# Kernel tuning notes

Measured on AMD Instinct MI355X. Metric: run time of the kernel, lower is better.

## Reference

```python
import jax, jax.numpy as jnp
from jax import lax
import numpy as np


def _conv2d(x, w, b, pad):
    # x: NCHW, w: OIHW
    o = lax.conv_general_dilated(x, w, window_strides=(1, 1),
                                 padding=[(pad, pad), (pad, pad)],
                                 dimension_numbers=('NCHW', 'OIHW', 'NCHW'))
    return o + b[None, :, None, None]


def _maxpool(x, kh, kw):
    return lax.reduce_window(x, -jnp.inf, lax.max,
                             window_dimensions=(1, 1, kh, kw),
                             window_strides=(1, 1, kh, kw),
                             padding='VALID')


def _l2norm(x, axis):
    n = jnp.sqrt(jnp.sum(x * x, axis=axis, keepdims=True))
    return x / jnp.maximum(n, 1e-12)


def setup_inputs() -> dict:
    key = jax.random.key(0)
    ks = jax.random.split(key, 12)
    d = {}
    d['x'] = jax.random.normal(ks[0], (16, 128, 40, 200), dtype=jnp.float32)
    d['cluster_centers'] = jax.random.uniform(ks[1], (64, 128), dtype=jnp.float32)
    d['conv_w'] = jax.random.normal(ks[2], (64, 128, 1, 1), dtype=jnp.float32) * 0.05
    d['conv_b'] = jax.random.normal(ks[3], (64,), dtype=jnp.float32) * 0.05
    d['w1'] = jax.random.normal(ks[4], (256, 128, 5, 5), dtype=jnp.float32) * 0.02
    d['b1'] = jax.random.normal(ks[5], (256,), dtype=jnp.float32) * 0.02
    d['w2'] = jax.random.normal(ks[6], (512, 256, 5, 5), dtype=jnp.float32) * 0.02
    d['b2'] = jax.random.normal(ks[7], (512,), dtype=jnp.float32) * 0.02
    d['w3'] = jax.random.normal(ks[8], (1024, 512, 5, 5), dtype=jnp.float32) * 0.02
    d['b3'] = jax.random.normal(ks[9], (1024,), dtype=jnp.float32) * 0.02
    d['mlp_w'] = jax.random.normal(ks[10], (256, 9216), dtype=jnp.float32) * 0.01
    d['mlp_b'] = jax.random.normal(ks[11], (256,), dtype=jnp.float32) * 0.01
    return d


def reference(x, cluster_centers, conv_w, conv_b, w1, b1, w2, b2, w3, b3, mlp_w, mlp_b):
    N, C, H, W = x.shape
    K = conv_w.shape[0]
    P = H * W

    # soft assignment: 1x1 conv -> softmax over cluster axis
    sa = _conv2d(x, conv_w, conv_b, 0).reshape(N, K, P)
    a = jax.nn.softmax(sa, axis=1)                      # [N, K, P]

    x_flat = x.reshape(N, C, P)
    # sum_p a[n,k,p] * (x[n,c,p] - centers[k,c])  -- algebraically equal to
    # the explicit NxKxCxP residual tensor, computed without materializing it.
    vlad = jnp.einsum('nkp,ncp->nkc', a, x_flat) \
           - a.sum(axis=-1)[:, :, None] * cluster_centers[None, :, :]
    vlad = _l2norm(vlad, axis=2)                        # intra-norm per cluster
    vlad = _l2norm(vlad.reshape(N, K * C), axis=1)      # [N, K*C]

    # CNN branch
    h = _conv2d(x, w1, b1, 2)
    h = jnp.where(h >= 0, h, 0.2 * h)                   # LeakyReLU(0.2)
    h = _maxpool(h, 2, 2)
    h = _conv2d(h, w2, b2, 2)
    h = jnp.where(h >= 0, h, 0.2 * h)
    h = _maxpool(h, 4, 4)
    h = _conv2d(h, w3, b3, 2)
    h = _maxpool(h, 5, 25)                              # -> [N, 1024, 1, 1]
    x_feat = _l2norm(h.reshape(N, -1), axis=1)          # [N, 1024]

    feat = jnp.concatenate([vlad, x_feat], axis=1)      # [N, 9216]
    out = feat @ mlp_w.T + mlp_b
    return _l2norm(out, axis=1)
```

## Files before the change

kernel.cpp:

```cpp
#include <hip/hip_runtime.h>
#include <math.h>

#define K_ 64
#define C_ 128
#define NB 16
#define P_ 8000

typedef float f32x4 __attribute__((ext_vector_type(4)));
typedef short s16x8 __attribute__((ext_vector_type(8)));

__device__ __forceinline__ short f2bf(float v) {
    unsigned u = __float_as_uint(v);
    u += 0x7FFFu + ((u >> 16) & 1u);
    return (short)(u >> 16);
}
__device__ __forceinline__ float bf2f(ushort u) { return __uint_as_float(((unsigned)u) << 16); }

__device__ __forceinline__ void stage16(const void* g, void* l) {
    __builtin_amdgcn_global_load_lds(
        (const __attribute__((address_space(1))) void*)g,
        (__attribute__((address_space(3))) void*)l, 16, 0, 0);
}

__global__ void k_transpose_tiled(const float* __restrict__ in, float* __restrict__ out,
                                  int Co, int E)
{
    __shared__ float t[32][33];
    const int e0  = blockIdx.x * 32;
    const int co0 = blockIdx.y * 32;
    for (int i = threadIdx.y; i < 32; i += 8) {
        int co = co0 + i, e = e0 + threadIdx.x;
        t[i][threadIdx.x] = (co < Co && e < E) ? in[(size_t)co * E + e] : 0.f;
    }
    __syncthreads();
    for (int i = threadIdx.y; i < 32; i += 8) {
        int e = e0 + i, co = co0 + threadIdx.x;
        if (e < E && co < Co) out[(size_t)e * Co + co] = t[threadIdx.x][i];
    }
}

__global__ void k_nchw_to_nhwc(const float* __restrict__ in, ushort* __restrict__ out,
                               int C, int P)
{
    __shared__ ushort t[32][33];
    const int n  = blockIdx.z;
    const int p0 = blockIdx.x * 32;
    const int c0 = blockIdx.y * 32;
    for (int i = threadIdx.y; i < 32; i += 8) {
        int c = c0 + i, p = p0 + threadIdx.x;
        t[i][threadIdx.x] = (c < C && p < P) ? (ushort)f2bf(in[((size_t)n * C + c) * P + p]) : 0;
    }
    __syncthreads();
    for (int i = threadIdx.y; i < 32; i += 8) {
        int p = p0 + i, c = c0 + threadIdx.x;
        if (p < P && c < C) out[((size_t)n * P + p) * C + c] = t[threadIdx.x][i];
    }
}

__global__ void k_wprep(const float* __restrict__ w, short* __restrict__ wb,
                        int Co, int Cin, int total)
{
    int idx = blockIdx.x * blockDim.x + threadIdx.x;
    if (idx >= total) return;
    int cl = idx & 31;
    int rest = idx >> 5;
    int co = rest % Co;
    int rest2 = rest / Co;
    int t = rest2 % 25;
    int ck = rest2 / 25;
    float v = w[((size_t)co * Cin + (ck << 5) + cl) * 25 + t];
    wb[idx] = f2bf(v);
}

template<int SR, int NC, int WR, int WC16, int IS3>
__global__ __launch_bounds__(256) void k_conv_mfma(
    const ushort* __restrict__ in, const s16x8* __restrict__ wb,
    const float* __restrict__ bias, ushort* __restrict__ outb, float* __restrict__ outf,
    const ushort* __restrict__ zg,
    int Cin, int Co, int H, int W, int WT, int leaky, int nck, int xpc, int PT)
{
    constexpr int NT   = IS3 ? 8 : (WR * WC16);
    constexpr int TOT  = SR * NC * 4;
    constexpr int TOTP = (TOT + 63) & ~63;
    __shared__ s16x8 xin[TOTP];

    const int tid  = threadIdx.x;
    const int lane = tid & 63;
    const int wid  = tid >> 6;
    const int wm   = wid;
    const int n16  = lane & 15;
    const int g    = lane >> 4;

    const int lid  = blockIdx.x;
    const int xcd  = lid & 7;
    const int rrr  = lid >> 3;
    const int co_blk = xcd / xpc;
    const int posn = rrr * xpc + (xcd % xpc);
    const int n    = posn / PT;
    const int bx   = posn % PT;

    const int h0  = IS3 ? 0 : (bx / WT) * WR;
    const int w0  = IS3 ? 0 : (bx % WT) * (WC16 * 16);
    const int ks  = IS3 ? bx : 0;
    const int co0 = co_blk * 256;

    int ph[NT], pw[NT];
    if (IS3) {
        #pragma unroll
        for (int nt = 0; nt < NT; ++nt) {
            int pos = nt * 16 + n16;
            int h = pos / 25;
            int w = pos - h * 25;
            if (h > 4) { h = 0; w = 0; }
            ph[nt] = h; pw[nt] = w;
        }
    }

    f32x4 acc[4][NT];
    #pragma unroll
    for (int i = 0; i < 4; ++i)
        #pragma unroll
        for (int j = 0; j < NT; ++j) acc[i][j] = f32x4{0.f, 0.f, 0.f, 0.f};

    const int ck0 = IS3 ? ks * nck : 0;
    const int ckend = ck0 + nck;

    auto stage_input = [&](int ck) {
        for (int c = wid; c * 64 < TOTP; c += 4) {
            int u = c * 64 + lane;
            int row = u / (NC * 4);
            int rem = u - row * (NC * 4);
            int col = rem >> 2;
            int s   = rem & 3;
            int g8  = (s - (col >> 1) - row) & 3;
            int gh = h0 + row - 2, gw = w0 + col - 2;
            const void* src =
                (u < TOT && (unsigned)gh < (unsigned)H && (unsigned)gw < (unsigned)W)
                ? (const void*)(in + ((size_t)(n * H + gh) * W + gw) * Cin + (ck << 5) + (g8 << 3))
                : (const void*)zg;
            stage16(src, (void*)&xin[c * 64]);
        }
    };

    for (int ck = ck0; ck < ckend; ++ck) {
        if (ck != ck0) __syncthreads();
        stage_input(ck);
        __syncthreads();

        const s16x8* wbc = wb + ((size_t)(ck * 25) * Co + co0 + wm * 64 + n16) * 4 + g;

        s16x8 wreg[3][4];
        #pragma unroll
        for (int mt = 0; mt < 4; ++mt) wreg[0][mt] = wbc[mt * 64];
        #pragma unroll
        for (int mt = 0; mt < 4; ++mt) wreg[1][mt] = wbc[(size_t)Co * 4 + mt * 64];

        #pragma unroll
        for (int t = 0; t < 25; ++t) {
            if (t < 23) {
                const s16x8* wn = wbc + (size_t)(t + 2) * Co * 4;
                #pragma unroll
                for (int mt = 0; mt < 4; ++mt) wreg[(t + 2) % 3][mt] = wn[mt * 64];
            }
            const int r = t / 5, s = t - (t / 5) * 5;

            s16x8 bf[NT];
            #pragma unroll
            for (int nt = 0; nt < NT; ++nt) {
                int row, col;
                if (IS3) { row = ph[nt] + r; col = pw[nt] + s; }
                else {
                    int rr = nt / WC16, cc = nt - rr * WC16;
                    row = rr + r;
                    col = cc * 16 + n16 + s;
                }
                bf[nt] = xin[(row * NC + col) * 4 + ((g + (col >> 1) + row) & 3)];
            }
            __builtin_amdgcn_s_setprio(1);
            #pragma unroll
            for (int mt = 0; mt < 4; ++mt)
                #pragma unroll
                for (int nt = 0; nt < NT; ++nt)
                    acc[mt][nt] = __builtin_amdgcn_mfma_f32_16x16x32_bf16(
                        wreg[t % 3][mt], bf[nt], acc[mt][nt], 0, 0, 0);
            __builtin_amdgcn_s_setprio(0);
        }
    }

    if (IS3) {
        #pragma unroll
        for (int mt = 0; mt < 4; ++mt) {
            #pragma unroll
            for (int reg = 0; reg < 4; ++reg) {
                const int co = co0 + wm * 64 + mt * 16 + g * 4 + reg;
                #pragma unroll
                for (int nt = 0; nt < NT; ++nt) {
                    int pos = nt * 16 + n16;
                    if (pos < 125)
                        outf[((size_t)(ks * NB + n) * Co + co) * 125 + pos] = acc[mt][nt][reg];
                }
            }
        }
    } else {
        #pragma unroll
        for (int mt = 0; mt < 4; ++mt) {
            const int cobase = co0 + wm * 64 + mt * 16 + g * 4;
            const float b0 = bias[cobase + 0];
            const float b1 = bias[cobase + 1];
            const float b2 = bias[cobase + 2];
            const float b3 = bias[cobase + 3];
            #pragma unroll
            for (int nt = 0; nt < NT; ++nt) {
                int rr = nt / WC16, cc = nt - rr * WC16;
                int h  = h0 + rr;
                int wp = w0 + cc * 16 + n16;
                if (h < H && wp < W) {
                    float v0 = acc[mt][nt][0] + b0;
                    float v1 = acc[mt][nt][1] + b1;
                    float v2 = acc[mt][nt][2] + b2;
                    float v3 = acc[mt][nt][3] + b3;
                    if (leaky) {
                        v0 = (v0 >= 0.f) ? v0 : 0.2f * v0;
                        v1 = (v1 >= 0.f) ? v1 : 0.2f * v1;
                        v2 = (v2 >= 0.f) ? v2 : 0.2f * v2;
                        v3 = (v3 >= 0.f) ? v3 : 0.2f * v3;
                    }
                    ushort4 pkd;
                    pkd.x = (ushort)f2bf(v0);
                    pkd.y = (ushort)f2bf(v1);
                    pkd.z = (ushort)f2bf(v2);
                    pkd.w = (ushort)f2bf(v3);
                    *(ushort4*)(outb + ((size_t)(n * H + h) * W + wp) * Co + cobase) = pkd;
                }
            }
        }
    }
}

__global__ __launch_bounds__(256) void k_vlad_partial(
    const float* __restrict__ x,
    const float* __restrict__ convw_t,
    const float* __restrict__ convb,
    float* __restrict__ pv,
    float* __restrict__ pa)
{
    __shared__ float xs[C_][64];
    __shared__ float als[64][K_];
    __shared__ float pgsum[4][K_];

    const int tid = threadIdx.x;
    const int chunk = blockIdx.x;
    const int n = blockIdx.y;
    const int p0 = chunk * 64;

    const float* xn = x + (size_t)n * C_ * P_ + p0;
    for (int i = tid; i < C_ * 64; i += 256) {
        int c = i >> 6, pp = i & 63;
        xs[c][pp] = xn[(size_t)c * P_ + pp];
    }
    __syncthreads();

    const int k  = tid & 63;
    const int pg = tid >> 6;

    float sa[16];
    const float bk = convb[k];
    #pragma unroll
    for (int j = 0; j < 16; ++j) sa[j] = bk;
    for (int c = 0; c < C_; ++c) {
        float wv = convw_t[c * K_ + k];
        const float4* xp = (const float4*)&xs[c][pg * 16];
        #pragma unroll
        for (int q = 0; q < 4; ++q) {
            float4 xv = xp[q];
            sa[q*4+0] += wv * xv.x;
            sa[q*4+1] += wv * xv.y;
            sa[q*4+2] += wv * xv.z;
            sa[q*4+3] += wv * xv.w;
        }
    }

    float asum_loc = 0.f;
    #pragma unroll
    for (int j = 0; j < 16; ++j) {
        float m = sa[j];
        for (int d = 32; d >= 1; d >>= 1) m = fmaxf(m, __shfl_xor(m, d));
        float e = __expf(sa[j] - m);
        float s = e;
        for (int d = 32; d >= 1; d >>= 1) s += __shfl_xor(s, d);
        float a = e / s;
        als[pg * 16 + j][k] = a;
        asum_loc += a;
    }
    pgsum[pg][k] = asum_loc;
    __syncthreads();
    if (tid < K_) {
        pa[((size_t)n * 125 + chunk) * K_ + tid] =
            pgsum[0][tid] + pgsum[1][tid] + pgsum[2][tid] + pgsum[3][tid];
    }

    const int q = pg;
    float acc[32];
    #pragma unroll
    for (int j = 0; j < 32; ++j) acc[j] = 0.f;
    for (int p = 0; p < 64; p += 4) {
        float a0 = als[p+0][k], a1 = als[p+1][k], a2 = als[p+2][k], a3 = als[p+3][k];
        #pragma unroll
        for (int j = 0; j < 32; ++j) {
            const float4 xv = *(const float4*)&xs[q*32 + j][p];
            acc[j] += a0*xv.x + a1*xv.y + a2*xv.z + a3*xv.w;
        }
    }
    float* pvp = pv + ((((size_t)n * 125 + chunk) * K_ + k) * C_ + q * 32);
    #pragma unroll
    for (int j = 0; j < 32; ++j) pvp[j] = acc[j];
}

__global__ void k_vlad_reduce(const float* __restrict__ pv, float* __restrict__ vlad_raw)
{
    int idx = blockIdx.x * blockDim.x + threadIdx.x;
    if (idx >= NB * 8192) return;
    int n = idx >> 13;
    int rest = idx & 8191;
    const float* p = pv + (size_t)n * 125 * 8192 + rest;
    float s = 0.f;
    for (int ch = 0; ch < 125; ++ch) s += p[(size_t)ch * 8192];
    vlad_raw[(size_t)n * 8192 + rest] = s;
}

__global__ void k_asum_reduce(const float* __restrict__ pa, float* __restrict__ asum)
{
    int idx = blockIdx.x * blockDim.x + threadIdx.x;
    if (idx >= NB * K_) return;
    const float* p = pa + (size_t)(idx >> 6) * 125 * K_ + (idx & 63);
    float s = 0.f;
    for (int ch = 0; ch < 125; ++ch) s += p[ch * K_];
    asum[idx] = s;
}

__global__ __launch_bounds__(128) void k_vlad_finalize(
    const float* __restrict__ vlad_raw, const float* __restrict__ asum,
    const float* __restrict__ centers, float* __restrict__ feat)
{
    __shared__ float red[2];
    const int k = blockIdx.x, n = blockIdx.y, c = threadIdx.x;
    float v = vlad_raw[((size_t)n * K_ + k) * C_ + c] - asum[n * K_ + k] * centers[k * C_ + c];
    float ss = v * v;
    for (int d = 32; d >= 1; d >>= 1) ss += __shfl_xor(ss, d);
    if ((threadIdx.x & 63) == 0) red[threadIdx.x >> 6] = ss;
    __syncthreads();
    float denom = fmaxf(sqrtf(red[0] + red[1]), 1e-12f);
    feat[(size_t)n * 9216 + k * C_ + c] = v / denom;
}

__global__ void k_maxpool_cl(const ushort* __restrict__ in, ushort* __restrict__ out,
                             int Hi, int Wi, int C8, int ph, int pw, int total)
{
    int idx = blockIdx.x * blockDim.x + threadIdx.x;
    if (idx >= total) return;
    const int Ho = Hi / ph, Wo = Wi / pw;
    const int C = C8 << 3;
    int c8 = idx % C8;
    int t  = idx / C8;
    int wo = t % Wo; t /= Wo;
    int ho = t % Ho;
    int n  = t / Ho;
    const ushort* base = in + ((size_t)(n * Hi + ho * ph) * Wi + wo * pw) * C + (c8 << 3);
    float m[8];
    #pragma unroll
    for (int j = 0; j < 8; ++j) m[j] = -INFINITY;
    for (int r = 0; r < ph; ++r)
        for (int s = 0; s < pw; ++s) {
            s16x8 v = *(const s16x8*)(base + ((size_t)r * Wi + s) * C);
            #pragma unroll
            for (int j = 0; j < 8; ++j) m[j] = fmaxf(m[j], bf2f((ushort)v[j]));
        }
    s16x8 o;
    #pragma unroll
    for (int j = 0; j < 8; ++j) o[j] = f2bf(m[j]);
    *(s16x8*)(out + ((size_t)(n * Ho + ho) * Wo + wo) * C + (c8 << 3)) = o;
}

__global__ void k_pool3_feat(const float* __restrict__ part, const float* __restrict__ bias,
                             float* __restrict__ feat)
{
    int idx = blockIdx.x * blockDim.x + threadIdx.x;
    if (idx >= NB * 1024) return;
    int n = idx >> 10, c = idx & 1023;
    const size_t kstride = (size_t)NB * 1024 * 125;
    const float* p = part + ((size_t)n * 1024 + c) * 125;
    const float b = bias[c];
    float m = -INFINITY;
    for (int i = 0; i < 125; ++i) {
        float s = 0.f;
        #pragma unroll
        for (int ksl = 0; ksl < 8; ++ksl) s += p[i + ksl * kstride];
        m = fmaxf(m, b + s);
    }
    feat[(size_t)n * 9216 + 8192 + c] = m;
}

__global__ __launch_bounds__(256) void k_featnorm(const float* __restrict__ feat,
                                                  float* __restrict__ scale)
{
    __shared__ float r1s[4], r2s[4];
    const int n = blockIdx.x;
    const int tid = threadIdx.x;
    const int wid = tid >> 6;
    float s1 = 0.f, s2 = 0.f;
    const float* f = feat + (size_t)n * 9216;
    for (int i = tid; i < 9216; i += 256) {
        float v = f[i];
        if (i < 8192) s1 += v * v; else s2 += v * v;
    }
    for (int d = 32; d >= 1; d >>= 1) { s1 += __shfl_xor(s1, d); s2 += __shfl_xor(s2, d); }
    if ((tid & 63) == 0) { r1s[wid] = s1; r2s[wid] = s2; }
    __syncthreads();
    if (tid == 0) {
        scale[n * 2 + 0] = 1.f / fmaxf(sqrtf(r1s[0] + r1s[1] + r1s[2] + r1s[3]), 1e-12f);
        scale[n * 2 + 1] = 1.f / fmaxf(sqrtf(r2s[0] + r2s[1] + r2s[2] + r2s[3]), 1e-12f);
    }
}

__global__ __launch_bounds__(256) void k_mlp_part(
    const float* __restrict__ feat, const float* __restrict__ scale,
    const float* __restrict__ wt,
    float* __restrict__ part)
{
    __shared__ float fs[576];
    const int n  = blockIdx.x >> 4;
    const int sl = blockIdx.x & 15;
    const int tid = threadIdx.x;
    const int base = sl * 576;
    for (int j = tid; j < 576; j += 256) {
        int idx = base + j;
        fs[j] = feat[(size_t)n * 9216 + idx] * scale[n * 2 + (idx < 8192 ? 0 : 1)];
    }
    __syncthreads();
    float a0 = 0.f, a1 = 0.f;
    for (int j = 0; j < 576; j += 2) {
        a0 += fs[j]     * wt[(size_t)(base + j)     * 256 + tid];
        a1 += fs[j + 1] * wt[(size_t)(base + j + 1) * 256 + tid];
    }
    part[((size_t)n * 16 + sl) * 256 + tid] = a0 + a1;
}

__global__ __launch_bounds__(256) void k_mlp_final(
    const float* __restrict__ part, const float* __restrict__ bias,
    float* __restrict__ outp)
{
    __shared__ float red[4];
    const int n = blockIdx.x;
    const int tid = threadIdx.x;
    float a = bias[tid];
    #pragma unroll
    for (int s = 0; s < 16; ++s) a += part[((size_t)n * 16 + s) * 256 + tid];
    float ss = a * a;
    for (int d = 32; d >= 1; d >>= 1) ss += __shfl_xor(ss, d);
    if ((tid & 63) == 0) red[tid >> 6] = ss;
    __syncthreads();
    const float inv = 1.f / fmaxf(sqrtf(red[0] + red[1] + red[2] + red[3]), 1e-12f);
    outp[n * 256 + tid] = a * inv;
}

extern "C" void kernel_launch(void* const* d_in, const int* in_sizes, int n_in,
                              void* d_out, int out_size, void* d_ws, size_t ws_size,
                              hipStream_t stream)
{
    const float* x      = (const float*)d_in[0];
    const float* cents  = (const float*)d_in[1];
    const float* conv_w = (const float*)d_in[2];
    const float* conv_b = (const float*)d_in[3];
    const float* w1     = (const float*)d_in[4];
    const float* b1     = (const float*)d_in[5];
    const float* w2     = (const float*)d_in[6];
    const float* b2     = (const float*)d_in[7];
    const float* w3     = (const float*)d_in[8];
    const float* b3     = (const float*)d_in[9];
    const float* mlp_w  = (const float*)d_in[10];
    const float* mlp_b  = (const float*)d_in[11];
    float* outp = (float*)d_out;

    char* ws = (char*)d_ws;
    size_t off = 0;
    auto alloc = [&](size_t bytes) -> void* {
        off = (off + 255) & ~(size_t)255;
        void* p = ws + off;
        off += bytes;
        return p;
    };
    ushort* zguard  = (ushort*)alloc(256);
    float*  convw_t = (float*)alloc((size_t)64 * 128 * 4);
    float*  mwt     = (float*)alloc((size_t)9216 * 256 * 4);
    short*  wb1     = (short*)alloc((size_t)819200 * 2);
    short*  wb2     = (short*)alloc((size_t)3276800 * 2);
    short*  wb3     = (short*)alloc((size_t)13107200 * 2);
    ushort* x_cl    = (ushort*)alloc((size_t)NB * 8000 * 128 * 2);
    float*  vlad_raw= (float*)alloc((size_t)NB * 8192 * 4);
    float*  asum    = (float*)alloc((size_t)NB * K_ * 4);
    float*  feat    = (float*)alloc((size_t)NB * 9216 * 4);
    float*  pa      = (float*)alloc((size_t)NB * 125 * K_ * 4);
    float*  scale   = (float*)alloc((size_t)NB * 2 * 4);
    float*  mpart   = (float*)alloc((size_t)NB * 16 * 256 * 4);
    ushort* pool2b  = (ushort*)alloc((size_t)NB * 125 * 512 * 2);
    char*   slabA   = (char*)alloc((size_t)8 * NB * 1024 * 125 * 4);
    ushort* slabB   = (ushort*)alloc((size_t)NB * 2000 * 256 * 2);

    hipMemsetAsync(zguard, 0, 256, stream);

    {
        dim3 blk(32, 8);
        k_transpose_tiled<<<dim3(4, 2), blk, 0, stream>>>(conv_w, convw_t, 64, 128);
        k_transpose_tiled<<<dim3(288, 8), blk, 0, stream>>>(mlp_w, mwt, 256, 9216);
        k_wprep<<<(819200 + 255) / 256, 256, 0, stream>>>(w1, wb1, 256, 128, 819200);
        k_wprep<<<(3276800 + 255) / 256, 256, 0, stream>>>(w2, wb2, 512, 256, 3276800);
        k_wprep<<<(13107200 + 255) / 256, 256, 0, stream>>>(w3, wb3, 1024, 512, 13107200);
        k_nchw_to_nhwc<<<dim3(250, 4, NB), blk, 0, stream>>>(x, x_cl, 128, 8000);
    }

    k_vlad_partial<<<dim3(125, NB), 256, 0, stream>>>(x, convw_t, conv_b, (float*)slabA, pa);
    k_vlad_reduce<<<(NB * 8192 + 255) / 256, 256, 0, stream>>>((float*)slabA, vlad_raw);
    k_asum_reduce<<<(NB * K_ + 255) / 256, 256, 0, stream>>>(pa, asum);
    k_vlad_finalize<<<dim3(K_, NB), 128, 0, stream>>>(vlad_raw, asum, cents, feat);

    k_conv_mfma<8, 36, 4, 2, 0><<<1120, 256, 0, stream>>>(
        x_cl, (const s16x8*)wb1, b1, (ushort*)slabA, nullptr, zguard,
        128, 256, 40, 200, 7, 1, 4, 8, 70);
    {
        int tot = NB * 20 * 100 * 32;
        k_maxpool_cl<<<(tot + 255) / 256, 256, 0, stream>>>(
            (ushort*)slabA, slabB, 40, 200, 32, 2, 2, tot);
    }
    k_conv_mfma<8, 36, 4, 2, 0><<<640, 256, 0, stream>>>(
        slabB, (const s16x8*)wb2, b2, (ushort*)slabA, nullptr, zguard,
        256, 512, 20, 100, 4, 1, 8, 4, 20);
    {
        int tot = NB * 5 * 25 * 64;
        k_maxpool_cl<<<(tot + 255) / 256, 256, 0, stream>>>(
            (ushort*)slabA, pool2b, 20, 100, 64, 4, 4, tot);
    }
    k_conv_mfma<9, 29, 4, 2, 1><<<512, 256, 0, stream>>>(
        pool2b, (const s16x8*)wb3, b3, nullptr, (float*)slabA, zguard,
        512, 1024, 5, 25, 1, 0, 2, 2, 8);
    k_pool3_feat<<<(NB * 1024 + 255) / 256, 256, 0, stream>>>((float*)slabA, b3, feat);

    k_featnorm<<<NB, 256, 0, stream>>>(feat, scale);
    k_mlp_part<<<NB * 16, 256, 0, stream>>>(feat, scale, mwt, mpart);
    k_mlp_final<<<NB, 256, 0, stream>>>(mpart, mlp_b, outp);
}
```

Before: 960.2 us.

## Split conv MFMA warps into 2x2 grid with 128 output channels each

Changes the per-wave tiling of the bf16 MFMA conv kernel. Each wave now covers 128 output channels by 4 spatial tiles instead of 64 channels by 8 tiles, arranged as a 2x2 grid of waves. The goal is to rebalance weight and LDS input fragment reuse, and the weight prefetch drops from a 3-deep ring to double buffering. NT is hardcoded to 4, so the tile shape is fixed and only correct if the template parameters match (WR=4, WC16=2). Register pressure rises because of 8x4 accumulators plus 16 weight fragments.

```diff
diff --git a/kernel.cpp b/kernel.cpp
--- a/kernel.cpp
+++ b/kernel.cpp
@@ -79,7 +79,7 @@
     const ushort* __restrict__ zg,
     int Cin, int Co, int H, int W, int WT, int leaky, int nck, int xpc, int PT)
 {
-    constexpr int NT   = IS3 ? 8 : (WR * WC16);
+    constexpr int NT   = 4;
     constexpr int TOT  = SR * NC * 4;
     constexpr int TOTP = (TOT + 63) & ~63;
     __shared__ s16x8 xin[TOTP];
@@ -87,7 +87,8 @@
     const int tid  = threadIdx.x;
     const int lane = tid & 63;
     const int wid  = tid >> 6;
-    const int wm   = wid;
+    const int wm   = wid >> 1;
+    const int wn   = wid & 1;
     const int n16  = lane & 15;
     const int g    = lane >> 4;
 
@@ -108,7 +109,7 @@
     if (IS3) {
         #pragma unroll
         for (int nt = 0; nt < NT; ++nt) {
-            int pos = nt * 16 + n16;
+            int pos = wn * 64 + nt * 16 + n16;
             int h = pos / 25;
             int w = pos - h * 25;
             if (h > 4) { h = 0; w = 0; }
@@ -116,9 +117,9 @@
         }
     }
 
-    f32x4 acc[4][NT];
-    #pragma unroll
-    for (int i = 0; i < 4; ++i)
+    f32x4 acc[8][NT];
+    #pragma unroll
+    for (int i = 0; i < 8; ++i)
         #pragma unroll
         for (int j = 0; j < NT; ++j) acc[i][j] = f32x4{0.f, 0.f, 0.f, 0.f};
 
@@ -147,20 +148,19 @@
         stage_input(ck);
         __syncthreads();
 
-        const s16x8* wbc = wb + ((size_t)(ck * 25) * Co + co0 + wm * 64 + n16) * 4 + g;
-
-        s16x8 wreg[3][4];
-        #pragma unroll
-        for (int mt = 0; mt < 4; ++mt) wreg[0][mt] = wbc[mt * 64];
-        #pragma unroll
-        for (int mt = 0; mt < 4; ++mt) wreg[1][mt] = wbc[(size_t)Co * 4 + mt * 64];
+        const s16x8* wbc = wb + ((size_t)(ck * 25) * Co + co0 + wm * 128 + n16) * 4 + g;
+
+        s16x8 wf[8];
+        #pragma unroll
+        for (int mt = 0; mt < 8; ++mt) wf[mt] = wbc[mt * 64];
 
         #pragma unroll
         for (int t = 0; t < 25; ++t) {
-            if (t < 23) {
-                const s16x8* wn = wbc + (size_t)(t + 2) * Co * 4;
+            s16x8 wfn[8];
+            if (t < 24) {
+                const s16x8* wnp = wbc + (size_t)(t + 1) * Co * 4;
                 #pragma unroll
-                for (int mt = 0; mt < 4; ++mt) wreg[(t + 2) % 3][mt] = wn[mt * 64];
+                for (int mt = 0; mt < 8; ++mt) wfn[mt] = wnp[mt * 64];
             }
             const int r = t / 5, s = t - (t / 5) * 5;
 
@@ -169,33 +169,33 @@
             for (int nt = 0; nt < NT; ++nt) {
                 int row, col;
                 if (IS3) { row = ph[nt] + r; col = pw[nt] + s; }
-                else {
-                    int rr = nt / WC16, cc = nt - rr * WC16;
-                    row = rr + r;
-                    col = cc * 16 + n16 + s;
-                }
+                else     { row = nt + r; col = wn * 16 + n16 + s; }
                 bf[nt] = xin[(row * NC + col) * 4 + ((g + (col >> 1) + row) & 3)];
             }
             __builtin_amdgcn_s_setprio(1);
             #pragma unroll
-            for (int mt = 0; mt < 4; ++mt)
+            for (int mt = 0; mt < 8; ++mt)
                 #pragma unroll
                 for (int nt = 0; nt < NT; ++nt)
                     acc[mt][nt] = __builtin_amdgcn_mfma_f32_16x16x32_bf16(
-                        wreg[t % 3][mt], bf[nt], acc[mt][nt], 0, 0, 0);
+                        wf[mt], bf[nt], acc[mt][nt], 0, 0, 0);
             __builtin_amdgcn_s_setprio(0);
+            if (t < 24) {
+                #pragma unroll
+                for (int mt = 0; mt < 8; ++mt) wf[mt] = wfn[mt];
+            }
         }
     }
 
     if (IS3) {
         #pragma unroll
-        for (int mt = 0; mt < 4; ++mt) {
+        for (int mt = 0; mt < 8; ++mt) {
             #pragma unroll
             for (int reg = 0; reg < 4; ++reg) {
-                const int co = co0 + wm * 64 + mt * 16 + g * 4 + reg;
+                const int co = co0 + wm * 128 + mt * 16 + g * 4 + reg;
                 #pragma unroll
                 for (int nt = 0; nt < NT; ++nt) {
-                    int pos = nt * 16 + n16;
+                    int pos = wn * 64 + nt * 16 + n16;
                     if (pos < 125)
                         outf[((size_t)(ks * NB + n) * Co + co) * 125 + pos] = acc[mt][nt][reg];
                 }
@@ -203,17 +203,16 @@
         }
     } else {
         #pragma unroll
-        for (int mt = 0; mt < 4; ++mt) {
-            const int cobase = co0 + wm * 64 + mt * 16 + g * 4;
-            const float b0 = bias[cobase + 0];
-            const float b1 = bias[cobase + 1];
-            const float b2 = bias[cobase + 2];
-            const float b3 = bias[cobase + 3];
+        for (int mt = 0; mt < 8; ++mt) {
+            const int cb = co0 + wm * 128 + mt * 16 + g * 4;
+            const float b0 = bias[cb + 0];
+            const float b1 = bias[cb + 1];
+            const float b2 = bias[cb + 2];
+            const float b3 = bias[cb + 3];
             #pragma unroll
             for (int nt = 0; nt < NT; ++nt) {
-                int rr = nt / WC16, cc = nt - rr * WC16;
-                int h  = h0 + rr;
-                int wp = w0 + cc * 16 + n16;
+                int h  = h0 + nt;
+                int wp = w0 + wn * 16 + n16;
                 if (h < H && wp < W) {
                     float v0 = acc[mt][nt][0] + b0;
                     float v1 = acc[mt][nt][1] + b1;
@@ -230,7 +229,7 @@
                     pkd.y = (ushort)f2bf(v1);
                     pkd.z = (ushort)f2bf(v2);
                     pkd.w = (ushort)f2bf(v3);
-                    *(ushort4*)(outb + ((size_t)(n * H + h) * W + wp) * Co + cobase) = pkd;
+                    *(ushort4*)(outb + ((size_t)(n * H + h) * W + wp) * Co + cb) = pkd;
                 }
             }
         }
```

Result: slower. 1.108 ms (+15.4%).

## Reorder conv tap loop to reuse LDS input fragments across kernel rows

Applied to the files above, without the earlier changes.

For the non-IS3 convolution path, the 25-tap loop becomes an outer loop over kernel columns. For each column, a strip of 8 rows x 2 column-tiles of input fragments is loaded from LDS once and reused across all 5 kernel rows, cutting LDS reads per tap. It also hardcodes NT=8 and a 4x2 output tile (WR=4, WC16=2), drops the 3-deep weight prefetch ring in favour of per-tap weight loads, and raises register pressure with 16 held fragments.

```diff
diff --git a/kernel.cpp b/kernel.cpp
--- a/kernel.cpp
+++ b/kernel.cpp
@@ -79,7 +79,7 @@
     const ushort* __restrict__ zg,
     int Cin, int Co, int H, int W, int WT, int leaky, int nck, int xpc, int PT)
 {
-    constexpr int NT   = IS3 ? 8 : (WR * WC16);
+    constexpr int NT   = 8;
     constexpr int TOT  = SR * NC * 4;
     constexpr int TOTP = (TOT + 63) & ~63;
     __shared__ s16x8 xin[TOTP];
@@ -149,41 +149,67 @@
 
         const s16x8* wbc = wb + ((size_t)(ck * 25) * Co + co0 + wm * 64 + n16) * 4 + g;
 
-        s16x8 wreg[3][4];
-        #pragma unroll
-        for (int mt = 0; mt < 4; ++mt) wreg[0][mt] = wbc[mt * 64];
-        #pragma unroll
-        for (int mt = 0; mt < 4; ++mt) wreg[1][mt] = wbc[(size_t)Co * 4 + mt * 64];
-
-        #pragma unroll
-        for (int t = 0; t < 25; ++t) {
-            if (t < 23) {
-                const s16x8* wn = wbc + (size_t)(t + 2) * Co * 4;
+        if constexpr (IS3) {
+            s16x8 wreg[3][4];
+            #pragma unroll
+            for (int mt = 0; mt < 4; ++mt) wreg[0][mt] = wbc[mt * 64];
+            #pragma unroll
+            for (int mt = 0; mt < 4; ++mt) wreg[1][mt] = wbc[(size_t)Co * 4 + mt * 64];
+
+            #pragma unroll
+            for (int t = 0; t < 25; ++t) {
+                if (t < 23) {
+                    const s16x8* wn = wbc + (size_t)(t + 2) * Co * 4;
+                    #pragma unroll
+                    for (int mt = 0; mt < 4; ++mt) wreg[(t + 2) % 3][mt] = wn[mt * 64];
+                }
+                const int r = t / 5, s = t - (t / 5) * 5;
+                s16x8 bf[NT];
                 #pragma unroll
-                for (int mt = 0; mt < 4; ++mt) wreg[(t + 2) % 3][mt] = wn[mt * 64];
+                for (int nt = 0; nt < NT; ++nt) {
+                    int row = ph[nt] + r, col = pw[nt] + s;
+                    bf[nt] = xin[(row * NC + col) * 4 + ((g + (col >> 1) + row) & 3)];
+                }
+                __builtin_amdgcn_s_setprio(1);
+                #pragma unroll
+                for (int mt = 0; mt < 4; ++mt)
+                    #pragma unroll
+                    for (int nt = 0; nt < NT; ++nt)
+                        acc[mt][nt] = __builtin_amdgcn_mfma_f32_16x16x32_bf16(
+                            wreg[t % 3][mt], bf[nt], acc[mt][nt], 0, 0, 0);
+                __builtin_amdgcn_s_setprio(0);
             }
-            const int r = t / 5, s = t - (t / 5) * 5;
-
-            s16x8 bf[NT];
-            #pragma unroll
-            for (int nt = 0; nt < NT; ++nt) {
-                int row, col;
-                if (IS3) { row = ph[nt] + r; col = pw[nt] + s; }
-                else {
-                    int rr = nt / WC16, cc = nt - rr * WC16;
-                    row = rr + r;
-                    col = cc * 16 + n16 + s;
+        } else {
+            #pragma unroll
+            for (int s = 0; s < 5; ++s) {
+                s16x8 bfs[16];
+                #pragma unroll
+                for (int row = 0; row < 8; ++row) {
+                    #pragma unroll
+                    for (int cc = 0; cc < 2; ++cc) {
+                        int col = cc * 16 + n16 + s;
+                        bfs[row * 2 + cc] =
+                            xin[(row * NC + col) * 4 + ((g + (col >> 1) + row) & 3)];
+                    }
                 }
-                bf[nt] = xin[(row * NC + col) * 4 + ((g + (col >> 1) + row) & 3)];
+                #pragma unroll
+                for (int r = 0; r < 5; ++r) {
+                    const s16x8* wp = wbc + (size_t)(r * 5 + s) * Co * 4;
+                    s16x8 wf[4];
+                    #pragma unroll
+                    for (int mt = 0; mt < 4; ++mt) wf[mt] = wp[mt * 64];
+                    __builtin_amdgcn_s_setprio(1);
+                    #pragma unroll
+                    for (int mt = 0; mt < 4; ++mt)
+                        #pragma unroll
+                        for (int nt = 0; nt < NT; ++nt) {
+                            const int rr = nt >> 1, cc = nt & 1;
+                            acc[mt][nt] = __builtin_amdgcn_mfma_f32_16x16x32_bf16(
+                                wf[mt], bfs[(rr + r) * 2 + cc], acc[mt][nt], 0, 0, 0);
+                        }
+                    __builtin_amdgcn_s_setprio(0);
+                }
             }
-            __builtin_amdgcn_s_setprio(1);
-            #pragma unroll
-            for (int mt = 0; mt < 4; ++mt)
-                #pragma unroll
-                for (int nt = 0; nt < NT; ++nt)
-                    acc[mt][nt] = __builtin_amdgcn_mfma_f32_16x16x32_bf16(
-                        wreg[t % 3][mt], bf[nt], acc[mt][nt], 0, 0, 0);
-            __builtin_amdgcn_s_setprio(0);
         }
     }
 
@@ -211,7 +237,7 @@
             const float b3 = bias[cobase + 3];
             #pragma unroll
             for (int nt = 0; nt < NT; ++nt) {
-                int rr = nt / WC16, cc = nt - rr * WC16;
+                int rr = nt >> 1, cc = nt & 1;
                 int h  = h0 + rr;
                 int wp = w0 + cc * 16 + n16;
                 if (h < H && wp < W) {
```

After: 1.170 ms. 21.8% more time.
